# Kernel tuning notes

Hardware: AMD Instinct MI355X
Metric: run time of the kernel (lower is better)

Reference implementation:

```python
import jax, jax.numpy as jnp
import numpy as np

EPS = 0.1        # init kwarg: eps
MAX_ITER = 50    # init kwarg: max_iter
EPS_LOG = 1e-8


def setup_inputs() -> dict:
    key = jax.random.key(0)
    k1, k2 = jax.random.split(key)
    x = jax.random.uniform(k1, (8, 2048, 2), dtype=jnp.float32)
    y = jax.random.uniform(k2, (8, 2048, 2), dtype=jnp.float32)
    return {"x": x, "y": y}


def _cost_matrix(x, y):
    # |x_i - y_j|^2 summed over feature dim -> (N, P, P)
    return jnp.sum(jnp.abs(x[:, :, None, :] - y[:, None, :, :]) ** 2, axis=-1)


def _M(C, u, v):
    # modified cost for log-domain updates: (-C + u_i + v_j) / eps
    return (-C + u[..., :, None] + v[..., None, :]) / EPS


def reference(x, y):
    mask = (x != -1).astype(x.dtype)
    x = x * mask
    y = y * mask

    C = _cost_matrix(x, y)  # (N, P, P)

    # marginals from squared second coordinate (detached in the original)
    a = x[:, :, 1] ** 2 / jnp.sum(x[:, :, 1] ** 2, axis=1, keepdims=True)
    b = y[:, :, 1] ** 2 / jnp.sum(y[:, :, 1] ** 2, axis=1, keepdims=True)
    mu = jax.lax.stop_gradient(a)
    nu = jax.lax.stop_gradient(b)

    u = jnp.zeros_like(mu)
    v = jnp.zeros_like(nu)

    def step(carry, _):
        u, v = carry
        u = EPS * (jnp.log(mu + EPS_LOG) - jax.nn.logsumexp(_M(C, u, v), axis=-1)) + u
        # logsumexp over transposed M == reduce over axis=-2
        v = EPS * (jnp.log(nu + EPS_LOG) - jax.nn.logsumexp(_M(C, u, v), axis=-2)) + v
        return (u, v), None

    (u, v), _ = jax.lax.scan(step, (u, v), None, length=MAX_ITER)

    pi = jnp.exp(_M(C, u, v))                 # transport plan (N, P, P)
    cost = jnp.sum(pi * C, axis=(-2, -1))     # (N,), reduction='none'
    return cost, pi, C
```

## Files before the change

kernel.cpp:

```cpp
#include <hip/hip_runtime.h>
#include <hip/hip_bf16.h>


#define P 2048
#define NB 8
constexpr float SCALE = 14.426950408889634f;

typedef float vf4 __attribute__((ext_vector_type(4)));

__global__ void setup_kernel(const float* __restrict__ x, const float* __restrict__ yy,
                             float4* __restrict__ jpackY, float4* __restrict__ jpackX,
                             float4* __restrict__ rowX, float4* __restrict__ rowY,
                             float* __restrict__ u, float* __restrict__ v,
                             float* __restrict__ partial) {
    const int n = blockIdx.x;
    const int t = threadIdx.x;
    __shared__ float redx[256], redy[256];
    float xm0[8], xm1[8], ym0[8], ym1[8];
    float sx = 0.f, sy = 0.f;
    #pragma unroll
    for (int k = 0; k < 8; ++k) {
        int p = t + 256 * k;
        size_t base = ((size_t)n * P + p) * 2;
        float a0 = x[base + 0];
        float a1 = x[base + 1];
        float b0 = yy[base + 0];
        float b1 = yy[base + 1];
        float m0 = (a0 != -1.0f) ? 1.0f : 0.0f;
        float m1 = (a1 != -1.0f) ? 1.0f : 0.0f;
        a0 *= m0; a1 *= m1; b0 *= m0; b1 *= m1;
        xm0[k] = a0; xm1[k] = a1; ym0[k] = b0; ym1[k] = b1;
        sx = fmaf(a1, a1, sx);
        sy = fmaf(b1, b1, sy);
    }
    redx[t] = sx; redy[t] = sy;
    __syncthreads();
    for (int off = 128; off > 0; off >>= 1) {
        if (t < off) { redx[t] += redx[t + off]; redy[t] += redy[t + off]; }
        __syncthreads();
    }
    const float inv_sx = 1.0f / redx[0];
    const float inv_sy = 1.0f / redy[0];
    #pragma unroll
    for (int k = 0; k < 8; ++k) {
        int p = t + 256 * k;
        float a0 = xm0[k], a1 = xm1[k], b0 = ym0[k], b1 = ym1[k];
        float qx = fmaf(a0, a0, a1 * a1);
        float qy = fmaf(b0, b0, b1 * b1);
        float mu = a1 * a1 * inv_sx;
        float nu = b1 * b1 * inv_sy;
        float Bmu = __builtin_amdgcn_logf(mu + 1e-8f) + SCALE * qx;
        float Bnu = __builtin_amdgcn_logf(nu + 1e-8f) + SCALE * qy;
        size_t idx = (size_t)n * P + p;
        rowX[idx] = make_float4(a0, a1, Bmu, 0.f);
        rowY[idx] = make_float4(b0, b1, Bnu, 0.f);
        jpackX[idx] = make_float4(2.f * SCALE * a0, 2.f * SCALE * a1, SCALE * qx, 0.f);
        jpackY[idx] = make_float4(2.f * SCALE * b0, 2.f * SCALE * b1, SCALE * qy, 0.f);
        u[idx] = 0.f;
        v[idx] = 0.f;
    }
    if (n == 0) { partial[t] = 0.f; partial[t + 256] = 0.f; }
}

__global__ __launch_bounds__(256, 2) void halfpass_kernel(
        const float4* __restrict__ jpack, const float* __restrict__ jdual,
        const float4* __restrict__ rowdat, float* __restrict__ outdual) {
    const int blk = blockIdx.x;
    const int batch = blk & 7;
    const int blkin = blk >> 3;
    const int lane = threadIdx.x & 63;
    const int wave = threadIdx.x >> 6;

    const float4* jp = jpack + (size_t)batch * P;
    const float* jd = jdual + (size_t)batch * P;

    float Y0[32], Y1[32], V[32];
    #pragma unroll
    for (int k = 0; k < 32; ++k) {
        int j = lane + 64 * k;
        float4 q = jp[j];
        float dv = jd[j];
        Y0[k] = q.x;
        Y1[k] = q.y;
        V[k] = dv - q.z;
    }

    const int rowbase = blkin * 32 + wave * 8;
    const float4* rd = rowdat + (size_t)batch * P;
    float* outp = outdual + (size_t)batch * P;

    for (int r = 0; r < 8; ++r) {
        const int i = rowbase + r;
        float4 rv = rd[i];
        const float x0 = rv.x, x1 = rv.y, B = rv.z;
        float a0 = 0.f, a1 = 0.f, a2 = 0.f, a3 = 0.f;
        #pragma unroll
        for (int k = 0; k < 32; k += 4) {
            a0 += __builtin_amdgcn_exp2f(fmaf(Y1[k + 0], x1, fmaf(Y0[k + 0], x0, V[k + 0])));
            a1 += __builtin_amdgcn_exp2f(fmaf(Y1[k + 1], x1, fmaf(Y0[k + 1], x0, V[k + 1])));
            a2 += __builtin_amdgcn_exp2f(fmaf(Y1[k + 2], x1, fmaf(Y0[k + 2], x0, V[k + 2])));
            a3 += __builtin_amdgcn_exp2f(fmaf(Y1[k + 3], x1, fmaf(Y0[k + 3], x0, V[k + 3])));
        }
        float acc = (a0 + a1) + (a2 + a3);
        #pragma unroll
        for (int m = 1; m < 64; m <<= 1) acc += __shfl_xor(acc, m, 64);
        if (lane == 0) outp[i] = B - __builtin_amdgcn_logf(acc);
    }
}

__global__ void final_kernel(const float4* __restrict__ rowX, const float4* __restrict__ rowY,
                             const float* __restrict__ u, const float* __restrict__ v,
                             float* __restrict__ out, float* __restrict__ partial) {
    const int blk = blockIdx.x;
    const int batch = blk & 7;
    const int i = blk >> 3;
    const int t = threadIdx.x;

    const float4 rx = rowX[(size_t)batch * P + i];
    const float ui = u[(size_t)batch * P + i];
    const float x0 = rx.x, x1 = rx.y;

    float* pi_out = out + 8 + (size_t)batch * P * P + (size_t)i * P;
    float* C_out = pi_out + (size_t)NB * P * P;
    const float4* ry = rowY + (size_t)batch * P;
    const float* vv = v + (size_t)batch * P;

    float costacc = 0.f;
    #pragma unroll
    for (int c = 0; c < 2; ++c) {
        const int j0 = c * 1024 + t * 4;
        vf4 vj = *(const vf4*)(vv + j0);
        vf4 Cv, Pv;
        #pragma unroll
        for (int e = 0; e < 4; ++e) {
            float4 q = ry[j0 + e];
            float dx = x0 - q.x;
            float dy = x1 - q.y;
            float Cj = fmaf(dy, dy, dx * dx);
            float pj = __builtin_amdgcn_exp2f(fmaf(Cj, -SCALE, ui + vj[e]));
            Cv[e] = Cj;
            Pv[e] = pj;
            costacc = fmaf(pj, Cj, costacc);
        }
        __builtin_nontemporal_store(Pv, (vf4*)(pi_out + j0));
        __builtin_nontemporal_store(Cv, (vf4*)(C_out + j0));
    }

    #pragma unroll
    for (int m = 1; m < 64; m <<= 1) costacc += __shfl_xor(costacc, m, 64);
    __shared__ float sred[4];
    const int wave = t >> 6, lane = t & 63;
    if (lane == 0) sred[wave] = costacc;
    __syncthreads();
    if (t == 0) {
        float s = sred[0] + sred[1] + sred[2] + sred[3];
        atomicAdd(&partial[batch * 64 + (i & 63)], s);
    }
}

__global__ void costreduce_kernel(const float* __restrict__ partial, float* __restrict__ out) {
    const int t = threadIdx.x;
    float val = partial[t];
    #pragma unroll
    for (int m = 1; m < 64; m <<= 1) val += __shfl_xor(val, m, 64);
    if ((t & 63) == 0) out[t >> 6] = val;
}

extern "C" void kernel_launch(void* const* d_in, const int* in_sizes, int n_in,
                              void* d_out, int out_size, void* d_ws, size_t ws_size,
                              hipStream_t stream) {
    const float* x = (const float*)d_in[0];
    const float* y = (const float*)d_in[1];
    float* out = (float*)d_out;
    float* ws = (float*)d_ws;

    float4* jpackY = (float4*)ws;
    float4* jpackX = (float4*)(ws + 65536);
    float4* rowX = (float4*)(ws + 131072);
    float4* rowY = (float4*)(ws + 196608);
    float* u = ws + 262144;
    float* v = ws + 262144 + 16384;
    float* partial = ws + 262144 + 32768;

    setup_kernel<<<8, 256, 0, stream>>>(x, y, jpackY, jpackX, rowX, rowY, u, v, partial);
    for (int it = 0; it < 50; ++it) {
        halfpass_kernel<<<512, 256, 0, stream>>>(jpackY, v, rowX, u);
        halfpass_kernel<<<512, 256, 0, stream>>>(jpackX, u, rowY, v);
    }
    final_kernel<<<16384, 256, 0, stream>>>(rowX, rowY, u, v, out, partial);
    costreduce_kernel<<<1, 512, 0, stream>>>(partial, out);
}
```

Measured before the change: 1.307 ms.

## Fuse Sinkhorn iterations into persistent kernel with per-batch grid barriers

Replaces the 100 separate half-pass kernel launches with one persistent kernel of 512 blocks that loops over all 50 iterations. Blocks of the same batch synchronise between half-passes through a per-batch flag array using release stores and acquire polling. This removes per-launch overhead and the tail drain between launches. It relies on all 512 blocks being co-resident (two blocks per CU under the launch bounds), otherwise the barrier can deadlock, and the spin-wait adds polling traffic.

Measured after the change: 3.393 ms. 2.6x slower.

```diff
diff --git a/kernel.cpp b/kernel.cpp
--- a/kernel.cpp
+++ b/kernel.cpp
@@ -12,7 +12,7 @@
                              float4* __restrict__ jpackY, float4* __restrict__ jpackX,
                              float4* __restrict__ rowX, float4* __restrict__ rowY,
                              float* __restrict__ u, float* __restrict__ v,
-                             float* __restrict__ partial) {
+                             float* __restrict__ partial, unsigned* __restrict__ flags) {
     const int n = blockIdx.x;
     const int t = threadIdx.x;
     __shared__ float redx[256], redy[256];
@@ -60,20 +60,32 @@
         v[idx] = 0.f;
     }
     if (n == 0) { partial[t] = 0.f; partial[t + 256] = 0.f; }
-}
-
-__global__ __launch_bounds__(256, 2) void halfpass_kernel(
-        const float4* __restrict__ jpack, const float* __restrict__ jdual,
-        const float4* __restrict__ rowdat, float* __restrict__ outdual) {
-    const int blk = blockIdx.x;
-    const int batch = blk & 7;
-    const int blkin = blk >> 3;
-    const int lane = threadIdx.x & 63;
-    const int wave = threadIdx.x >> 6;
-
-    const float4* jp = jpack + (size_t)batch * P;
-    const float* jd = jdual + (size_t)batch * P;
-
+    if (t < 64) flags[n * 64 + t] = 0u;
+}
+
+__device__ __forceinline__ void batch_barrier(unsigned* __restrict__ bflags,
+                                              const int blkin, const unsigned stamp) {
+    __syncthreads();
+    if (threadIdx.x < 64) {
+        if (threadIdx.x == 0)
+            __hip_atomic_store(&bflags[blkin], stamp, __ATOMIC_RELEASE,
+                               __HIP_MEMORY_SCOPE_AGENT);
+        while (true) {
+            unsigned f = __hip_atomic_load(&bflags[threadIdx.x], __ATOMIC_RELAXED,
+                                           __HIP_MEMORY_SCOPE_AGENT);
+            if (__all((int)(f >= stamp))) break;
+            __builtin_amdgcn_s_sleep(1);
+        }
+        __builtin_amdgcn_fence(__ATOMIC_ACQUIRE, "agent");
+    }
+    __syncthreads();
+}
+
+__device__ __forceinline__ void halfpass_dev(const float4* __restrict__ jp,
+                                             const float* __restrict__ jd,
+                                             const float4* __restrict__ rd,
+                                             float* __restrict__ outp,
+                                             const int lane, const int rowbase) {
     float Y0[32], Y1[32], V[32];
     #pragma unroll
     for (int k = 0; k < 32; ++k) {
@@ -84,11 +96,7 @@
         Y1[k] = q.y;
         V[k] = dv - q.z;
     }
-
-    const int rowbase = blkin * 32 + wave * 8;
-    const float4* rd = rowdat + (size_t)batch * P;
-    float* outp = outdual + (size_t)batch * P;
-
+    #pragma unroll 1
     for (int r = 0; r < 8; ++r) {
         const int i = rowbase + r;
         float4 rv = rd[i];
@@ -105,6 +113,36 @@
         #pragma unroll
         for (int m = 1; m < 64; m <<= 1) acc += __shfl_xor(acc, m, 64);
         if (lane == 0) outp[i] = B - __builtin_amdgcn_logf(acc);
+    }
+}
+
+__global__ __launch_bounds__(256, 2) void sinkhorn_persist(
+        const float4* __restrict__ jpackY, const float4* __restrict__ jpackX,
+        const float4* __restrict__ rowX, const float4* __restrict__ rowY,
+        float* __restrict__ u, float* __restrict__ v,
+        unsigned* __restrict__ flags) {
+    const int blk = blockIdx.x;
+    const int batch = blk & 7;
+    const int blkin = blk >> 3;
+    const int lane = threadIdx.x & 63;
+    const int wave = threadIdx.x >> 6;
+    const int rowbase = blkin * 32 + wave * 8;
+
+    const size_t boff = (size_t)batch * P;
+    const float4* jpY = jpackY + boff;
+    const float4* jpX = jpackX + boff;
+    const float4* rX = rowX + boff;
+    const float4* rY = rowY + boff;
+    float* ub = u + boff;
+    float* vb = v + boff;
+    unsigned* bflags = flags + batch * 64;
+
+    unsigned stamp = 1u;
+    for (int it = 0; it < 50; ++it) {
+        halfpass_dev(jpY, vb, rX, ub, lane, rowbase);
+        batch_barrier(bflags, blkin, stamp++);
+        halfpass_dev(jpX, ub, rY, vb, lane, rowbase);
+        if (it < 49) batch_barrier(bflags, blkin, stamp++);
     }
 }
 
@@ -181,12 +219,11 @@
     float* u = ws + 262144;
     float* v = ws + 262144 + 16384;
     float* partial = ws + 262144 + 32768;
-
-    setup_kernel<<<8, 256, 0, stream>>>(x, y, jpackY, jpackX, rowX, rowY, u, v, partial);
-    for (int it = 0; it < 50; ++it) {
-        halfpass_kernel<<<512, 256, 0, stream>>>(jpackY, v, rowX, u);
-        halfpass_kernel<<<512, 256, 0, stream>>>(jpackX, u, rowY, v);
-    }
+    unsigned* flags = (unsigned*)(ws + 262144 + 32768 + 512);
+
+    setup_kernel<<<8, 256, 0, stream>>>(x, y, jpackY, jpackX, rowX, rowY, u, v,
+                                        partial, flags);
+    sinkhorn_persist<<<512, 256, 0, stream>>>(jpackY, jpackX, rowX, rowY, u, v, flags);
     final_kernel<<<16384, 256, 0, stream>>>(rowX, rowY, u, v, out, partial);
     costreduce_kernel<<<1, 512, 0, stream>>>(partial, out);
 }
```
